# Performance work log

Hardware: AMD Instinct MI355X
Metric: run time of the kernel (lower is better)

The kernel has to match this reference:

```python
import jax, jax.numpy as jnp
import numpy as np

N_LAYERS = 4
D_MODEL = 1024
D_INNER = 2048
DT_RANK = 64
D_STATE = 16
D_CONV = 4
EPS = 1e-5


def _rms(x, w):
    return x * jax.lax.rsqrt(jnp.mean(x * x, axis=-1, keepdims=True) + EPS) * w


def _silu(x):
    return x * jax.nn.sigmoid(x)


def setup_inputs() -> dict:
    key = jax.random.key(0)
    ks = jax.random.split(key, 8)
    B, L = 2, 1024
    s = 0.02
    nl, dm, di = N_LAYERS, D_MODEL, D_INNER
    return {
        "x": jax.random.normal(ks[0], (B, L, dm), dtype=jnp.float32),
        "norm_w": jnp.ones((nl, dm), dtype=jnp.float32),
        "W_in": jax.random.normal(ks[1], (nl, 2 * di, dm), dtype=jnp.float32) * s,
        "conv_w": jax.random.normal(ks[2], (nl, di, D_CONV), dtype=jnp.float32) * s,
        "conv_b": jnp.zeros((nl, di), dtype=jnp.float32),
        "W_x": jax.random.normal(ks[3], (nl, DT_RANK + 2 * D_STATE, di), dtype=jnp.float32) * s,
        "W_dt": jax.random.normal(ks[4], (nl, di, DT_RANK), dtype=jnp.float32) * (DT_RANK ** -0.5),
        "b_dt": jax.random.normal(ks[5], (nl, di), dtype=jnp.float32) - 3.0,  # softplus -> small dt, like inv-softplus init
        "A_log": jax.random.uniform(ks[6], (nl, di, D_STATE), dtype=jnp.float32) * 2.0,  # A = -exp(A_log) in [-7.4, -1]
        "D": jnp.ones((nl, di), dtype=jnp.float32),
        "W_out": jax.random.normal(ks[7], (nl, dm, di), dtype=jnp.float32) * s,
    }


def reference(x, norm_w, W_in, conv_w, conv_b, W_x, W_dt, b_dt, A_log, D, W_out):
    nl = W_in.shape[0]
    L = x.shape[1]
    dc = conv_w.shape[-1]
    n = A_log.shape[-1]
    rk = W_dt.shape[-1]

    def combine(left, right):
        a1, b1 = left
        a2, b2 = right
        return a2 * a1, a2 * b1 + b2

    for i in range(nl):
        h = _rms(x, norm_w[i])
        xz = jnp.einsum('bld,ed->ble', h, W_in[i])          # [B,L,2*Di]
        xi, z = jnp.split(xz, 2, axis=-1)
        # causal depthwise conv1d (padding=dc-1, keep first L outputs)
        xp = jnp.pad(xi, ((0, 0), (dc - 1, 0), (0, 0)))
        xc = conv_b[i] + sum(xp[:, k:k + L, :] * conv_w[i][:, k] for k in range(dc))
        xc = _silu(xc)
        # SSM parameterization
        dbc = jnp.einsum('bld,ed->ble', xc, W_x[i])          # [B,L,rk+2n]
        delta, Bm, Cm = jnp.split(dbc, [rk, rk + n], axis=-1)
        delta = jax.nn.softplus(jnp.einsum('blr,dr->bld', delta, W_dt[i]) + b_dt[i])  # [B,L,Di]
        A = -jnp.exp(A_log[i])                               # [Di,N]
        deltaA = jnp.exp(delta[..., None] * A)               # [B,L,Di,N]
        BX = (delta * xc)[..., None] * Bm[:, :, None, :]     # [B,L,Di,N]
        # parallel scan: h_t = deltaA_t * h_{t-1} + BX_t
        _, hs = jax.lax.associative_scan(combine, (deltaA, BX), axis=1)
        y = jnp.einsum('bldn,bln->bld', hs, Cm) + D[i] * xc
        out = jnp.einsum('bld,ed->ble', y * _silu(z), W_out[i])
        x = x + out
    return x
```

## Files before the change

### kernel.cpp

```cpp
#include <hip/hip_runtime.h>
#include <hip/hip_bf16.h>
#include <math.h>

#define NL 4
#define DM 1024
#define DI 2048
#define RK 64
#define NS 16
#define LSEQ 1024
#define BATCH 2
#define MROWS (BATCH*LSEQ)
#define NCHUNK 32
#define LC 32

typedef __attribute__((ext_vector_type(8))) short bf16x8;
typedef __attribute__((ext_vector_type(4))) float f32x4;

__device__ __forceinline__ float bf2f(unsigned short u){
  union { unsigned int i; float f; } v; v.i = ((unsigned int)u) << 16; return v.f;
}
__device__ __forceinline__ unsigned short f2bf(float f){
  union { float f; unsigned int i; } v; v.f = f;
  unsigned int r = v.i + 0x7fffu + ((v.i >> 16) & 1u);
  return (unsigned short)(r >> 16);
}
__device__ __forceinline__ float sigmoidf_(float x){ return 1.0f / (1.0f + __expf(-x)); }
__device__ __forceinline__ float softplusf_(float x){ return (x > 20.0f) ? x : log1pf(__expf(x)); }

__device__ __forceinline__ void gl2lds16(const void* g, void* l) {
  __builtin_amdgcn_global_load_lds((__attribute__((address_space(1))) void*)g,
                                   (__attribute__((address_space(3))) void*)l,
                                   16, 0, 0);
}

template<int BM, int BN, int WAVES_M, int WAVES_N, int EPI>
__global__ __launch_bounds__(256)
void gemm_bt(const unsigned short* __restrict__ A, const unsigned short* __restrict__ W,
             void* __restrict__ C, const float* __restrict__ bias,
             int M, int N, int K, int ldc, int kslices)
{
  constexpr int MT = BM / (WAVES_M * 16);
  constexpr int NT = BN / (WAVES_N * 16);
  __shared__ __align__(16) unsigned short As[BM * 32];
  __shared__ __align__(16) unsigned short Bs[BN * 32];

  const int tid  = threadIdx.x;
  const int wave = tid >> 6;
  const int lane = tid & 63;
  const int wm   = wave / WAVES_N;
  const int wn   = wave % WAVES_N;
  const int quad = lane >> 4;
  const int l16  = lane & 15;
  const int srow = lane >> 2;
  const int scol = (lane & 3) * 8;

  const int m0 = blockIdx.x * BM;
  const int n0 = blockIdx.y * BN;
  const int Ks = K / kslices;
  const int kb = blockIdx.z * Ks;

  f32x4 acc[MT][NT];
  #pragma unroll
  for (int i = 0; i < MT; i++)
    #pragma unroll
    for (int j = 0; j < NT; j++)
      acc[i][j] = (f32x4){0.f, 0.f, 0.f, 0.f};

  for (int k0 = kb; k0 < kb + Ks; k0 += 32) {
    const unsigned short* Ab = A + (size_t)m0 * K + k0;
    for (int c = wave; c < BM / 16; c += 4)
      gl2lds16(Ab + (size_t)(c * 16 + srow) * K + scol, As + c * 512);
    const unsigned short* Wb = W + (size_t)n0 * K + k0;
    for (int c = wave; c < BN / 16; c += 4)
      gl2lds16(Wb + (size_t)(c * 16 + srow) * K + scol, Bs + c * 512);
    __syncthreads();

    bf16x8 af[MT], bfr[NT];
    #pragma unroll
    for (int mt = 0; mt < MT; mt++)
      af[mt] = *(const bf16x8*)(As + (wm * MT * 16 + mt * 16 + l16) * 32 + quad * 8);
    #pragma unroll
    for (int nt = 0; nt < NT; nt++)
      bfr[nt] = *(const bf16x8*)(Bs + (wn * NT * 16 + nt * 16 + l16) * 32 + quad * 8);
    #pragma unroll
    for (int mt = 0; mt < MT; mt++)
      #pragma unroll
      for (int nt = 0; nt < NT; nt++)
        acc[mt][nt] = __builtin_amdgcn_mfma_f32_16x16x32_bf16(af[mt], bfr[nt], acc[mt][nt], 0, 0, 0);
    __syncthreads();
  }

  #pragma unroll
  for (int mt = 0; mt < MT; mt++) {
    #pragma unroll
    for (int nt = 0; nt < NT; nt++) {
      int n = n0 + wn * NT * 16 + nt * 16 + l16;
      #pragma unroll
      for (int r = 0; r < 4; r++) {
        int m = m0 + wm * MT * 16 + mt * 16 + quad * 4 + r;
        float v = acc[mt][nt][r];
        size_t off = (size_t)m * ldc + n;
        if constexpr (EPI == 0)      ((unsigned short*)C)[off] = f2bf(v);
        else if constexpr (EPI == 1) atomicAdd((float*)C + off, v);
        else if constexpr (EPI == 2) ((float*)C)[off] = softplusf_(v + bias[n]);
        else if constexpr (EPI == 3) ((float*)C)[off] += v;
        else                         ((float*)C)[off] = v;
      }
    }
  }
}

__global__ __launch_bounds__(256)
void rmsnorm_kernel(const float* __restrict__ x, const float* __restrict__ w,
                    unsigned short* __restrict__ h)
{
  const int row = blockIdx.x;
  const float4 a = ((const float4*)(x + (size_t)row * DM))[threadIdx.x];
  float ss = a.x*a.x + a.y*a.y + a.z*a.z + a.w*a.w;
  #pragma unroll
  for (int o = 32; o > 0; o >>= 1) ss += __shfl_down(ss, o);
  __shared__ float red[4];
  if ((threadIdx.x & 63) == 0) red[threadIdx.x >> 6] = ss;
  __syncthreads();
  float rs = rsqrtf((red[0] + red[1] + red[2] + red[3]) * (1.0f / DM) + 1e-5f);
  const float4 wv = ((const float4*)w)[threadIdx.x];
  ushort4 o4;
  o4.x = f2bf(a.x * rs * wv.x);
  o4.y = f2bf(a.y * rs * wv.y);
  o4.z = f2bf(a.z * rs * wv.z);
  o4.w = f2bf(a.w * rs * wv.w);
  ((ushort4*)(h + (size_t)row * DM))[threadIdx.x] = o4;
}

__global__ __launch_bounds__(256)
void conv_silu_kernel(const unsigned short* __restrict__ xz,
                      const float* __restrict__ cw, const float* __restrict__ cb,
                      unsigned short* __restrict__ xc)
{
  int idx = blockIdx.x * 256 + threadIdx.x;
  int d = idx & (DI - 1);
  int t = (idx >> 11) & (LSEQ - 1);
  int b = idx >> 21;
  const float4 w4 = ((const float4*)cw)[d];
  const float wk[4] = {w4.x, w4.y, w4.z, w4.w};
  const unsigned short* xi = xz + (size_t)b * LSEQ * (2 * DI) + d;
  float acc = cb[d];
  #pragma unroll
  for (int k = 0; k < 4; k++) {
    int tt = t - 3 + k;
    if (tt >= 0) acc += bf2f(xi[(size_t)tt * (2 * DI)]) * wk[k];
  }
  xc[idx] = f2bf(acc * sigmoidf_(acc));
}

__global__ __launch_bounds__(256)
void extract_dt_kernel(const float* __restrict__ dbc, unsigned short* __restrict__ out)
{
  int idx = blockIdx.x * 256 + threadIdx.x;
  int m = idx >> 6, r = idx & 63;
  out[idx] = f2bf(dbc[(size_t)m * 96 + r]);
}

__global__ void f32_to_bf16_kernel(const float* __restrict__ s, unsigned short* __restrict__ d, int n4)
{
  int i = blockIdx.x * 256 + threadIdx.x;
  int stride = gridDim.x * 256;
  for (; i < n4; i += stride) {
    float4 v = ((const float4*)s)[i];
    ushort4 o; o.x = f2bf(v.x); o.y = f2bf(v.y); o.z = f2bf(v.z); o.w = f2bf(v.w);
    ((ushort4*)d)[i] = o;
  }
}

__global__ __launch_bounds__(256)
void scan1_kernel(const float* __restrict__ delta, const unsigned short* __restrict__ xc,
                  const float* __restrict__ dbc, const float* __restrict__ A_log,
                  float* __restrict__ hend, float* __restrict__ sumd)
{
  const int d = blockIdx.x * 256 + threadIdx.x;
  const int c = blockIdx.y;
  const int b = blockIdx.z;
  const int t0 = c * LC;
  __shared__ float bc[LC][32];
  #pragma unroll
  for (int i = 0; i < (LC * 32) / 256; i++) {
    int f = i * 256 + threadIdx.x;
    int r = f >> 5, col = f & 31;
    bc[r][col] = dbc[(size_t)(b * LSEQ + t0 + r) * 96 + 64 + col];
  }
  float Av[NS], h[NS];
  #pragma unroll
  for (int n = 0; n < NS; n++) { Av[n] = -__expf(A_log[(size_t)d * NS + n]); h[n] = 0.f; }
  __syncthreads();
  float sd = 0.f;
  for (int t = 0; t < LC; t++) {
    size_t ix = (size_t)(b * LSEQ + t0 + t) * DI + d;
    float dt = delta[ix];
    float xcv = bf2f(xc[ix]);
    sd += dt;
    float dx = dt * xcv;
    #pragma unroll
    for (int n = 0; n < NS; n++) {
      float da = __expf(dt * Av[n]);
      h[n] = da * h[n] + dx * bc[t][n];
    }
  }
  size_t base = ((size_t)(b * NCHUNK + c) * NS) * DI + d;
  #pragma unroll
  for (int n = 0; n < NS; n++) hend[base + (size_t)n * DI] = h[n];
  sumd[(size_t)(b * NCHUNK + c) * DI + d] = sd;
}

__global__ __launch_bounds__(256)
void scan2_kernel(const float* __restrict__ A_log, const float* __restrict__ hend,
                  const float* __restrict__ sumd, float* __restrict__ hin)
{
  int g = blockIdx.x * 256 + threadIdx.x;
  int b = g >> 11;
  int d = g & (DI - 1);
  float Av[NS], H[NS];
  #pragma unroll
  for (int n = 0; n < NS; n++) { Av[n] = -__expf(A_log[(size_t)d * NS + n]); H[n] = 0.f; }
  for (int c = 0; c < NCHUNK; c++) {
    size_t base = ((size_t)(b * NCHUNK + c) * NS) * DI + d;
    float sd = sumd[(size_t)(b * NCHUNK + c) * DI + d];
    #pragma unroll
    for (int n = 0; n < NS; n++) {
      hin[base + (size_t)n * DI] = H[n];
      float da = __expf(Av[n] * sd);
      H[n] = da * H[n] + hend[base + (size_t)n * DI];
    }
  }
}

__global__ __launch_bounds__(256)
void scan3_kernel(const float* __restrict__ delta, const unsigned short* __restrict__ xc,
                  const float* __restrict__ dbc, const float* __restrict__ A_log,
                  const float* __restrict__ hin, const float* __restrict__ Dvec,
                  const unsigned short* __restrict__ xz, unsigned short* __restrict__ g)
{
  const int d = blockIdx.x * 256 + threadIdx.x;
  const int c = blockIdx.y;
  const int b = blockIdx.z;
  const int t0 = c * LC;
  __shared__ float bc[LC][32];
  #pragma unroll
  for (int i = 0; i < (LC * 32) / 256; i++) {
    int f = i * 256 + threadIdx.x;
    int r = f >> 5, col = f & 31;
    bc[r][col] = dbc[(size_t)(b * LSEQ + t0 + r) * 96 + 64 + col];
  }
  float Av[NS], h[NS];
  size_t base = ((size_t)(b * NCHUNK + c) * NS) * DI + d;
  #pragma unroll
  for (int n = 0; n < NS; n++) {
    Av[n] = -__expf(A_log[(size_t)d * NS + n]);
    h[n] = hin[base + (size_t)n * DI];
  }
  const float Dd = Dvec[d];
  __syncthreads();
  for (int t = 0; t < LC; t++) {
    size_t ix = (size_t)(b * LSEQ + t0 + t) * DI + d;
    float dt = delta[ix];
    float xcv = bf2f(xc[ix]);
    float dx = dt * xcv;
    float y = Dd * xcv;
    #pragma unroll
    for (int n = 0; n < NS; n++) {
      float da = __expf(dt * Av[n]);
      h[n] = da * h[n] + dx * bc[t][n];
      y += h[n] * bc[t][16 + n];
    }
    float zv = bf2f(xz[(size_t)(b * LSEQ + t0 + t) * (2 * DI) + DI + d]);
    g[ix] = f2bf(y * (zv * sigmoidf_(zv)));
  }
}

extern "C" void kernel_launch(void* const* d_in, const int* in_sizes, int n_in,
                              void* d_out, int out_size, void* d_ws, size_t ws_size,
                              hipStream_t stream)
{
  const float* x_in   = (const float*)d_in[0];
  const float* norm_w = (const float*)d_in[1];
  const float* W_in   = (const float*)d_in[2];
  const float* conv_w = (const float*)d_in[3];
  const float* conv_b = (const float*)d_in[4];
  const float* W_x    = (const float*)d_in[5];
  const float* W_dt   = (const float*)d_in[6];
  const float* b_dt   = (const float*)d_in[7];
  const float* A_log  = (const float*)d_in[8];
  const float* Dv     = (const float*)d_in[9];
  const float* W_out  = (const float*)d_in[10];
  float* x = (float*)d_out;

  char* p = (char*)d_ws;
  auto alloc = [&](size_t bytes) {
    void* r = (void*)p;
    p += (bytes + 255) & ~(size_t)255;
    return r;
  };
  unsigned short* Win_bf  = (unsigned short*)alloc((size_t)NL * 2 * DI * DM * 2);
  unsigned short* Wx_bf   = (unsigned short*)alloc((size_t)NL * 96 * DI * 2);
  unsigned short* Wdt_bf  = (unsigned short*)alloc((size_t)NL * DI * RK * 2);
  unsigned short* Wout_bf = (unsigned short*)alloc((size_t)NL * DM * DI * 2);
  unsigned short* h_bf    = (unsigned short*)alloc((size_t)MROWS * DM * 2);
  unsigned short* xz_bf   = (unsigned short*)alloc((size_t)MROWS * 2 * DI * 2);
  unsigned short* xc_bf   = (unsigned short*)alloc((size_t)MROWS * DI * 2);
  float*          dbc     = (float*)alloc((size_t)MROWS * 96 * 4);
  unsigned short* dt_bf   = (unsigned short*)alloc((size_t)MROWS * RK * 2);
  float*          delta   = (float*)alloc((size_t)MROWS * DI * 4);
  unsigned short* g_bf    = (unsigned short*)alloc((size_t)MROWS * DI * 2);
  float*          hend    = (float*)alloc((size_t)BATCH * NCHUNK * NS * DI * 4);
  float*          hin     = (float*)alloc((size_t)BATCH * NCHUNK * NS * DI * 4);
  float*          sumd    = (float*)alloc((size_t)BATCH * NCHUNK * DI * 4);

  hipMemcpyAsync(x, x_in, (size_t)MROWS * DM * 4, hipMemcpyDeviceToDevice, stream);

  f32_to_bf16_kernel<<<2048, 256, 0, stream>>>(W_in,  Win_bf,  NL * 2 * DI * DM / 4);
  f32_to_bf16_kernel<<<256,  256, 0, stream>>>(W_x,   Wx_bf,   NL * 96 * DI / 4);
  f32_to_bf16_kernel<<<256,  256, 0, stream>>>(W_dt,  Wdt_bf,  NL * DI * RK / 4);
  f32_to_bf16_kernel<<<1024, 256, 0, stream>>>(W_out, Wout_bf, NL * DM * DI / 4);

  for (int l = 0; l < NL; l++) {
    const unsigned short* Win_l  = Win_bf  + (size_t)l * 2 * DI * DM;
    const unsigned short* Wx_l   = Wx_bf   + (size_t)l * 96 * DI;
    const unsigned short* Wdt_l  = Wdt_bf  + (size_t)l * DI * RK;
    const unsigned short* Wout_l = Wout_bf + (size_t)l * DM * DI;

    rmsnorm_kernel<<<MROWS, 256, 0, stream>>>(x, norm_w + (size_t)l * DM, h_bf);

    gemm_bt<128, 128, 2, 2, 0><<<dim3(MROWS / 128, (2 * DI) / 128), 256, 0, stream>>>(
        h_bf, Win_l, xz_bf, nullptr, MROWS, 2 * DI, DM, 2 * DI, 1);

    conv_silu_kernel<<<(BATCH * LSEQ * DI) / 256, 256, 0, stream>>>(
        xz_bf, conv_w + (size_t)l * DI * 4, conv_b + (size_t)l * DI, xc_bf);

    hipMemsetAsync(dbc, 0, (size_t)MROWS * 96 * 4, stream);
    gemm_bt<64, 96, 4, 1, 1><<<dim3(MROWS / 64, 1, 4), 256, 0, stream>>>(
        xc_bf, Wx_l, dbc, nullptr, MROWS, 96, DI, 96, 4);

    extract_dt_kernel<<<(MROWS * RK) / 256, 256, 0, stream>>>(dbc, dt_bf);

    gemm_bt<128, 128, 2, 2, 2><<<dim3(MROWS / 128, DI / 128), 256, 0, stream>>>(
        dt_bf, Wdt_l, delta, b_dt + (size_t)l * DI, MROWS, DI, RK, DI, 1);

    scan1_kernel<<<dim3(DI / 256, NCHUNK, BATCH), 256, 0, stream>>>(
        delta, xc_bf, dbc, A_log + (size_t)l * DI * NS, hend, sumd);
    scan2_kernel<<<(BATCH * DI) / 256, 256, 0, stream>>>(
        A_log + (size_t)l * DI * NS, hend, sumd, hin);
    scan3_kernel<<<dim3(DI / 256, NCHUNK, BATCH), 256, 0, stream>>>(
        delta, xc_bf, dbc, A_log + (size_t)l * DI * NS, hin, Dv + (size_t)l * DI, xz_bf, g_bf);

    gemm_bt<128, 128, 2, 2, 1><<<dim3(MROWS / 128, DM / 128, 4), 256, 0, stream>>>(
        g_bf, Wout_l, x, nullptr, MROWS, DM, DI, DM, 4);
  }
}
```

Measured before the change: 946.1 us.

## Double GEMM K-tile with XOR-swizzled LDS and replace atomics with split-K reduce kernels

The GEMM K step grows from 32 to 64, and the LDS layout gets an XOR swizzle to avoid bank conflicts. This halves the number of barriers per K. The split-K atomicAdd epilogues are replaced by per-slice partial buffers (aliased onto the delta buffer) plus dedicated reduce kernels, and the memset and extract_dt kernel go away. The four weight-conversion launches are merged into one kernel. The cost is more LDS per block and extra partial-buffer traffic. Aliasing part buffers onto delta relies on stream ordering.

```diff
diff --git a/kernel.cpp b/kernel.cpp
--- a/kernel.cpp
+++ b/kernel.cpp
@@ -41,8 +41,8 @@
 {
   constexpr int MT = BM / (WAVES_M * 16);
   constexpr int NT = BN / (WAVES_N * 16);
-  __shared__ __align__(16) unsigned short As[BM * 32];
-  __shared__ __align__(16) unsigned short Bs[BN * 32];
+  __shared__ __align__(16) unsigned short As[BM * 64];
+  __shared__ __align__(16) unsigned short Bs[BN * 64];
 
   const int tid  = threadIdx.x;
   const int wave = tid >> 6;
@@ -51,8 +51,8 @@
   const int wn   = wave % WAVES_N;
   const int quad = lane >> 4;
   const int l16  = lane & 15;
-  const int srow = lane >> 2;
-  const int scol = (lane & 3) * 8;
+  const int srow = lane >> 3;
+  const int scol = ((lane & 7) ^ srow) * 8;
 
   const int m0 = blockIdx.x * BM;
   const int n0 = blockIdx.y * BN;
@@ -66,30 +66,44 @@
     for (int j = 0; j < NT; j++)
       acc[i][j] = (f32x4){0.f, 0.f, 0.f, 0.f};
 
-  for (int k0 = kb; k0 < kb + Ks; k0 += 32) {
+  for (int k0 = kb; k0 < kb + Ks; k0 += 64) {
     const unsigned short* Ab = A + (size_t)m0 * K + k0;
-    for (int c = wave; c < BM / 16; c += 4)
-      gl2lds16(Ab + (size_t)(c * 16 + srow) * K + scol, As + c * 512);
+    #pragma unroll
+    for (int i = 0; i < BM / 32; i++) {
+      int c = i * 4 + wave;
+      gl2lds16(Ab + (size_t)(c * 8 + srow) * K + scol, As + c * 512);
+    }
     const unsigned short* Wb = W + (size_t)n0 * K + k0;
-    for (int c = wave; c < BN / 16; c += 4)
-      gl2lds16(Wb + (size_t)(c * 16 + srow) * K + scol, Bs + c * 512);
+    #pragma unroll
+    for (int i = 0; i < BN / 32; i++) {
+      int c = i * 4 + wave;
+      gl2lds16(Wb + (size_t)(c * 8 + srow) * K + scol, Bs + c * 512);
+    }
     __syncthreads();
 
-    bf16x8 af[MT], bfr[NT];
-    #pragma unroll
-    for (int mt = 0; mt < MT; mt++)
-      af[mt] = *(const bf16x8*)(As + (wm * MT * 16 + mt * 16 + l16) * 32 + quad * 8);
-    #pragma unroll
-    for (int nt = 0; nt < NT; nt++)
-      bfr[nt] = *(const bf16x8*)(Bs + (wn * NT * 16 + nt * 16 + l16) * 32 + quad * 8);
-    #pragma unroll
-    for (int mt = 0; mt < MT; mt++)
+    #pragma unroll
+    for (int h = 0; h < 2; h++) {
+      bf16x8 af[MT], bfr[NT];
       #pragma unroll
-      for (int nt = 0; nt < NT; nt++)
-        acc[mt][nt] = __builtin_amdgcn_mfma_f32_16x16x32_bf16(af[mt], bfr[nt], acc[mt][nt], 0, 0, 0);
+      for (int mt = 0; mt < MT; mt++) {
+        int rA = wm * MT * 16 + mt * 16 + l16;
+        af[mt] = *(const bf16x8*)(As + rA * 64 + (((h * 4 + quad) ^ (rA & 7)) << 3));
+      }
+      #pragma unroll
+      for (int nt = 0; nt < NT; nt++) {
+        int rB = wn * NT * 16 + nt * 16 + l16;
+        bfr[nt] = *(const bf16x8*)(Bs + rB * 64 + (((h * 4 + quad) ^ (rB & 7)) << 3));
+      }
+      #pragma unroll
+      for (int mt = 0; mt < MT; mt++)
+        #pragma unroll
+        for (int nt = 0; nt < NT; nt++)
+          acc[mt][nt] = __builtin_amdgcn_mfma_f32_16x16x32_bf16(af[mt], bfr[nt], acc[mt][nt], 0, 0, 0);
+    }
     __syncthreads();
   }
 
+  const size_t slice_off = (size_t)blockIdx.z * M * ldc;
   #pragma unroll
   for (int mt = 0; mt < MT; mt++) {
     #pragma unroll
@@ -101,13 +115,40 @@
         float v = acc[mt][nt][r];
         size_t off = (size_t)m * ldc + n;
         if constexpr (EPI == 0)      ((unsigned short*)C)[off] = f2bf(v);
-        else if constexpr (EPI == 1) atomicAdd((float*)C + off, v);
         else if constexpr (EPI == 2) ((float*)C)[off] = softplusf_(v + bias[n]);
-        else if constexpr (EPI == 3) ((float*)C)[off] += v;
-        else                         ((float*)C)[off] = v;
+        else                         ((float*)C)[slice_off + off] = v;
       }
     }
   }
+}
+
+__global__ __launch_bounds__(256)
+void reduce4_kernel(const float* __restrict__ part, float* __restrict__ x)
+{
+  const size_t MN = (size_t)MROWS * DM;
+  int i = blockIdx.x * 256 + threadIdx.x;
+  float4 a = ((const float4*)part)[i];
+  float4 b = ((const float4*)(part + MN))[i];
+  float4 c = ((const float4*)(part + 2 * MN))[i];
+  float4 d = ((const float4*)(part + 3 * MN))[i];
+  float4 o = ((float4*)x)[i];
+  o.x += a.x + b.x + c.x + d.x;
+  o.y += a.y + b.y + c.y + d.y;
+  o.z += a.z + b.z + c.z + d.z;
+  o.w += a.w + b.w + c.w + d.w;
+  ((float4*)x)[i] = o;
+}
+
+__global__ __launch_bounds__(256)
+void reduce2_kernel(const float* __restrict__ part, float* __restrict__ dbc,
+                    unsigned short* __restrict__ dt_bf)
+{
+  const int MN = MROWS * 96;
+  int i = blockIdx.x * 256 + threadIdx.x;
+  float v = part[i] + part[MN + i] + part[2 * MN + i] + part[3 * MN + i];
+  dbc[i] = v;
+  int m = i / 96, c = i - m * 96;
+  if (c < RK) dt_bf[m * RK + c] = f2bf(v);
 }
 
 __global__ __launch_bounds__(256)
@@ -153,22 +194,21 @@
   xc[idx] = f2bf(acc * sigmoidf_(acc));
 }
 
-__global__ __launch_bounds__(256)
-void extract_dt_kernel(const float* __restrict__ dbc, unsigned short* __restrict__ out)
-{
-  int idx = blockIdx.x * 256 + threadIdx.x;
-  int m = idx >> 6, r = idx & 63;
-  out[idx] = f2bf(dbc[(size_t)m * 96 + r]);
-}
-
-__global__ void f32_to_bf16_kernel(const float* __restrict__ s, unsigned short* __restrict__ d, int n4)
-{
-  int i = blockIdx.x * 256 + threadIdx.x;
-  int stride = gridDim.x * 256;
-  for (; i < n4; i += stride) {
-    float4 v = ((const float4*)s)[i];
-    ushort4 o; o.x = f2bf(v.x); o.y = f2bf(v.y); o.z = f2bf(v.z); o.w = f2bf(v.w);
-    ((ushort4*)d)[i] = o;
+__global__ void convert_all_kernel(const float* __restrict__ W_in, unsigned short* __restrict__ Win_bf,
+                                   const float* __restrict__ W_x,  unsigned short* __restrict__ Wx_bf,
+                                   const float* __restrict__ W_dt, unsigned short* __restrict__ Wdt_bf,
+                                   const float* __restrict__ W_out,unsigned short* __restrict__ Wout_bf)
+{
+  const float* src[4]  = {W_in, W_x, W_dt, W_out};
+  unsigned short* dst[4] = {Win_bf, Wx_bf, Wdt_bf, Wout_bf};
+  const int n4[4] = {NL*2*DI*DM/4, NL*96*DI/4, NL*DI*RK/4, NL*DM*DI/4};
+  for (int s = 0; s < 4; s++) {
+    int stride = gridDim.x * 256;
+    for (int i = blockIdx.x * 256 + threadIdx.x; i < n4[s]; i += stride) {
+      float4 v = ((const float4*)src[s])[i];
+      ushort4 o; o.x = f2bf(v.x); o.y = f2bf(v.y); o.z = f2bf(v.z); o.w = f2bf(v.w);
+      ((ushort4*)dst[s])[i] = o;
+    }
   }
 }
 
@@ -308,18 +348,18 @@
   unsigned short* xc_bf   = (unsigned short*)alloc((size_t)MROWS * DI * 2);
   float*          dbc     = (float*)alloc((size_t)MROWS * 96 * 4);
   unsigned short* dt_bf   = (unsigned short*)alloc((size_t)MROWS * RK * 2);
+  unsigned short* g_bf    = (unsigned short*)alloc((size_t)MROWS * DI * 2);
   float*          delta   = (float*)alloc((size_t)MROWS * DI * 4);
-  unsigned short* g_bf    = (unsigned short*)alloc((size_t)MROWS * DI * 2);
   float*          hend    = (float*)alloc((size_t)BATCH * NCHUNK * NS * DI * 4);
   float*          hin     = (float*)alloc((size_t)BATCH * NCHUNK * NS * DI * 4);
   float*          sumd    = (float*)alloc((size_t)BATCH * NCHUNK * DI * 4);
+  float* part2 = delta;
+  float* part4 = delta;
 
   hipMemcpyAsync(x, x_in, (size_t)MROWS * DM * 4, hipMemcpyDeviceToDevice, stream);
 
-  f32_to_bf16_kernel<<<2048, 256, 0, stream>>>(W_in,  Win_bf,  NL * 2 * DI * DM / 4);
-  f32_to_bf16_kernel<<<256,  256, 0, stream>>>(W_x,   Wx_bf,   NL * 96 * DI / 4);
-  f32_to_bf16_kernel<<<256,  256, 0, stream>>>(W_dt,  Wdt_bf,  NL * DI * RK / 4);
-  f32_to_bf16_kernel<<<1024, 256, 0, stream>>>(W_out, Wout_bf, NL * DM * DI / 4);
+  convert_all_kernel<<<2048, 256, 0, stream>>>(W_in, Win_bf, W_x, Wx_bf,
+                                               W_dt, Wdt_bf, W_out, Wout_bf);
 
   for (int l = 0; l < NL; l++) {
     const unsigned short* Win_l  = Win_bf  + (size_t)l * 2 * DI * DM;
@@ -335,11 +375,9 @@
     conv_silu_kernel<<<(BATCH * LSEQ * DI) / 256, 256, 0, stream>>>(
         xz_bf, conv_w + (size_t)l * DI * 4, conv_b + (size_t)l * DI, xc_bf);
 
-    hipMemsetAsync(dbc, 0, (size_t)MROWS * 96 * 4, stream);
-    gemm_bt<64, 96, 4, 1, 1><<<dim3(MROWS / 64, 1, 4), 256, 0, stream>>>(
-        xc_bf, Wx_l, dbc, nullptr, MROWS, 96, DI, 96, 4);
-
-    extract_dt_kernel<<<(MROWS * RK) / 256, 256, 0, stream>>>(dbc, dt_bf);
+    gemm_bt<64, 96, 4, 1, 4><<<dim3(MROWS / 64, 1, 4), 256, 0, stream>>>(
+        xc_bf, Wx_l, part2, nullptr, MROWS, 96, DI, 96, 4);
+    reduce2_kernel<<<(MROWS * 96) / 256, 256, 0, stream>>>(part2, dbc, dt_bf);
 
     gemm_bt<128, 128, 2, 2, 2><<<dim3(MROWS / 128, DI / 128), 256, 0, stream>>>(
         dt_bf, Wdt_l, delta, b_dt + (size_t)l * DI, MROWS, DI, RK, DI, 1);
@@ -351,7 +389,8 @@
     scan3_kernel<<<dim3(DI / 256, NCHUNK, BATCH), 256, 0, stream>>>(
         delta, xc_bf, dbc, A_log + (size_t)l * DI * NS, hin, Dv + (size_t)l * DI, xz_bf, g_bf);
 
-    gemm_bt<128, 128, 2, 2, 1><<<dim3(MROWS / 128, DM / 128, 4), 256, 0, stream>>>(
-        g_bf, Wout_l, x, nullptr, MROWS, DM, DI, DM, 4);
-  }
-}
+    gemm_bt<128, 128, 2, 2, 4><<<dim3(MROWS / 128, DM / 128, 4), 256, 0, stream>>>(
+        g_bf, Wout_l, part4, nullptr, MROWS, DM, DI, DM, 4);
+    reduce4_kernel<<<(MROWS * DM) / 1024, 256, 0, stream>>>(part4, x);
+  }
+}
```

Measured after the change: 959.0 us. About the same (+1.4%).
